# Performance work log

Hardware: AMD Instinct MI355X
Metric: run time of the kernel (lower is better)

The kernel has to match this reference:

```python
import jax, jax.numpy as jnp
import numpy as np

EPS = 1e-7  # SimplifiedLayerNorm eps


def setup_inputs() -> dict:
    key = jax.random.key(0)
    k1, k2 = jax.random.split(key)
    x = jax.random.normal(k1, (8, 2048, 64), dtype=jnp.float32)   # [B, T, d]
    W = jax.random.normal(k2, (2048, 8), dtype=jnp.float32)       # [T, H] per-distance, per-head Toeplitz weights
    return {"x": x, "W": W}


def _l2norm(v):
    return v / (jnp.linalg.norm(v, axis=-1, keepdims=True) + EPS)


def reference(x, W):
    B, T, d = x.shape
    H = W.shape[1]
    # pad one zero token: [B, T+1, d]
    xp = jnp.concatenate([x, jnp.zeros((B, 1, d), x.dtype)], axis=1)
    idx = jnp.arange(T + 1)
    dist = idx[:, None] - idx[None, :]                 # [T+1, T+1], row - col
    # Toeplitz logits: W[dist, h] for 0 <= dist < T; the single dist==T entry
    # (bottom-left corner) is left at its initial 0.0; dist < 0 is causally masked.
    Wd = W[jnp.clip(dist, 0, T - 1)]                   # [T+1, T+1, H]
    dist3 = dist[..., None]
    logits = jnp.where(dist3 < 0, -jnp.inf,
                       jnp.where(dist3 >= T, jnp.zeros((), x.dtype), Wd))
    probs = jax.nn.softmax(logits, axis=1)             # softmax over columns (dim=-1 of W_h)
    v = jnp.einsum('tsh,bsd->hbtd', probs, xp)         # [H, B, T+1, d]
    v = _l2norm(v)
    V = jnp.concatenate([v, xp[None]], axis=0)         # [H+1, B, T+1, d]
    V = _l2norm(V)
    return V
```

## Files before the change

### kernel.cpp

```cpp
#include <hip/hip_runtime.h>

#define EPS 1e-7f
#define T_DIM 2048
#define TP1   2049
#define H_DIM 8
#define B_DIM 8
#define SP    2080
#define NFRAG 134
#define FB_OFF 32
#define RSTRIDE 66

typedef short v8s __attribute__((ext_vector_type(8)));
typedef float v4f __attribute__((ext_vector_type(4)));

static __device__ __forceinline__ unsigned short f2bf(float f) {
  union { float f; unsigned u; } v; v.f = f;
  unsigned r = v.u + 0x7fffu + ((v.u >> 16) & 1u);
  return (unsigned short)(r >> 16);
}

#define J1_BLOCKS 268
#define J2_BLOCKS 264
#define J3_BLOCKS 4098

__global__ __launch_bounds__(256) void prep(const float* __restrict__ x,
                                            const float* __restrict__ W,
                                            unsigned short* __restrict__ fragA,
                                            unsigned short* __restrict__ xT,
                                            float* __restrict__ out) {
  __shared__ float tile[64][65];
  int bid = blockIdx.x;
  if (bid < J1_BLOCKS) {
    int tid = bid * 256 + threadIdx.x;
    int blk = tid >> 6, lane = tid & 63;
    int h = blk / NFRAG, fb = blk - h * NFRAG;
    int b0 = fb * 16 - FB_OFF;
    int lm = lane & 15, quad = lane >> 4;
    v8s frag;
    #pragma unroll
    for (int j = 0; j < 8; ++j) {
      int d = b0 + lm - 8 * quad - j;
      float v = 0.0f;
      if (d >= 0 && d < T_DIM) v = __expf(W[d * H_DIM + h]);
      else if (d == T_DIM) v = 1.0f;
      frag[j] = (short)f2bf(v);
    }
    *(v8s*)(fragA + (size_t)tid * 8) = frag;
    return;
  }
  bid -= J1_BLOCKS;
  if (bid < J2_BLOCKS) {
    int b = bid / 33, st = bid % 33;
    int tid = threadIdx.x;
    if (st == 32) {
      #pragma unroll
      for (int i = 0; i < 8; ++i) {
        int idx = tid * 8 + i;
        int dd = idx >> 5, sl = idx & 31;
        xT[((size_t)b * 64 + dd) * SP + T_DIM + sl] = 0;
      }
      return;
    }
    int s0 = st * 64;
    int c = tid & 63, r4 = tid >> 6;
    #pragma unroll
    for (int i = 0; i < 16; ++i) {
      int sl = r4 * 16 + i;
      tile[sl][c] = x[((size_t)b * T_DIM + (s0 + sl)) * 64 + c];
    }
    __syncthreads();
    #pragma unroll
    for (int i = 0; i < 16; ++i) {
      int dd = r4 * 16 + i;
      xT[((size_t)b * 64 + dd) * SP + s0 + c] = f2bf(tile[c][dd]);
    }
    return;
  }
  bid -= J2_BLOCKS;
  {
    int row = bid * 4 + (threadIdx.x >> 6);
    if (row >= B_DIM * TP1) return;
    int b = row / TP1, t = row - b * TP1;
    int dd = threadIdx.x & 63;
    float v = (t < T_DIM) ? x[((size_t)b * T_DIM + t) * 64 + dd] : 0.0f;
    float ss = v * v;
    ss += __shfl_xor(ss, 1);  ss += __shfl_xor(ss, 2);
    ss += __shfl_xor(ss, 4);  ss += __shfl_xor(ss, 8);
    ss += __shfl_xor(ss, 16); ss += __shfl_xor(ss, 32);
    float inv = 1.0f / (sqrtf(ss) + EPS);
    out[(((size_t)(H_DIM * B_DIM + b) * TP1 + t) << 6) + dd] = v * inv;
  }
}

__global__ __launch_bounds__(256) void toeplitz_mm(const unsigned short* __restrict__ fragA,
                                                   const unsigned short* __restrict__ xT,
                                                   float* __restrict__ out) {
  __shared__ float bufA[64 * RSTRIDE];
  __shared__ float bufB[64 * RSTRIDE];

  const int lane = threadIdx.x & 63;
  const int w    = threadIdx.x >> 6;
  const int lm   = lane & 15;
  const int quad = lane >> 4;

  const int bi  = blockIdx.x;
  const int tt  = 32 - (bi >> 6);
  const int rem = bi & 63;
  const int h = rem >> 3, b = rem & 7;
  const int t0 = tt * 64;

  const unsigned short* fA = fragA + ((size_t)h * NFRAG * 64 + lane) * 8;
  const unsigned short* xb = xT + ((size_t)b * 64 + lm) * SP + 8 * quad;

  const int s_end = min(t0 + 32, T_DIM);

  v4f acc[4][4] = {};

  v8s a0[4], a1[4], b0[4], b1[4];

#define LOAD_A(dst, s0v) do {                                        \
    const v8s* _p = (const v8s*)(fA + (size_t)(((t0 - (s0v) + FB_OFF) >> 4)) * 512); \
    dst[0] = _p[0]; dst[1] = _p[64]; dst[2] = _p[128]; dst[3] = _p[192]; } while (0)
#define LOAD_B(dst, s0v) do {                                        \
    const unsigned short* _p = xb + (s0v);                           \
    dst[0] = *(const v8s*)(_p);                                      \
    dst[1] = *(const v8s*)(_p + 16 * SP);                            \
    dst[2] = *(const v8s*)(_p + 32 * SP);                            \
    dst[3] = *(const v8s*)(_p + 48 * SP); } while (0)
#define DO_MFMA(fa, fb) do {                                         \
    _Pragma("unroll")                                                \
    for (int mt = 0; mt < 4; ++mt)                                   \
      _Pragma("unroll")                                              \
      for (int nt = 0; nt < 4; ++nt)                                 \
        acc[mt][nt] = __builtin_amdgcn_mfma_f32_16x16x32_bf16(fa[mt], fb[nt], acc[mt][nt], 0, 0, 0); } while (0)

  int s0 = 32 * w;
  if (s0 <= s_end) {
    LOAD_A(a0, s0); LOAD_B(b0, s0);
    for (;;) {
      bool more = (s0 + 128 <= s_end);
      if (more) { LOAD_A(a1, s0 + 128); LOAD_B(b1, s0 + 128); }
      DO_MFMA(a0, b0);
      if (!more) break;
      s0 += 128;
      bool more2 = (s0 + 128 <= s_end);
      if (more2) { LOAD_A(a0, s0 + 128); LOAD_B(b0, s0 + 128); }
      DO_MFMA(a1, b1);
      if (!more2) break;
      s0 += 128;
    }
  }

#define ST_ACC(buf) do {                                             \
    _Pragma("unroll")                                                \
    for (int mt = 0; mt < 4; ++mt)                                   \
      _Pragma("unroll")                                              \
      for (int r = 0; r < 4; ++r) {                                  \
        int row = 16 * mt + 4 * quad + r;                            \
        _Pragma("unroll")                                            \
        for (int nt = 0; nt < 4; ++nt)                               \
          buf[row * RSTRIDE + 16 * nt + lm] = acc[mt][nt][r]; } } while (0)
#define ADD_ACC(buf) do {                                            \
    _Pragma("unroll")                                                \
    for (int mt = 0; mt < 4; ++mt)                                   \
      _Pragma("unroll")                                              \
      for (int r = 0; r < 4; ++r) {                                  \
        int row = 16 * mt + 4 * quad + r;                            \
        _Pragma("unroll")                                            \
        for (int nt = 0; nt < 4; ++nt)                               \
          acc[mt][nt][r] += buf[row * RSTRIDE + 16 * nt + lm]; } } while (0)

  if (w == 1) ST_ACC(bufA);
  if (w == 3) ST_ACC(bufB);
  __syncthreads();
  if (w == 0) ADD_ACC(bufA);
  if (w == 2) ADD_ACC(bufB);
  __syncthreads();
  if (w == 2) ST_ACC(bufA);
  __syncthreads();
  if (w != 0) return;
  ADD_ACC(bufA);

  #pragma unroll
  for (int mt = 0; mt < 4; ++mt) {
    #pragma unroll
    for (int r = 0; r < 4; ++r) {
      float ss = 0.0f;
      #pragma unroll
      for (int nt = 0; nt < 4; ++nt) { float a = acc[mt][nt][r]; ss += a * a; }
      ss += __shfl_xor(ss, 1);
      ss += __shfl_xor(ss, 2);
      ss += __shfl_xor(ss, 4);
      ss += __shfl_xor(ss, 8);
      int t = t0 + 16 * mt + 4 * quad + r;
      if (t <= T_DIM) {
        float n1 = sqrtf(ss);
        float u  = n1 / (n1 + EPS);
        float inv = 1.0f / ((n1 + EPS) * (u + EPS));
        float* op = out + (((size_t)(h * B_DIM + b) * TP1 + t) << 6) + lm;
        #pragma unroll
        for (int nt = 0; nt < 4; ++nt) op[16 * nt] = acc[mt][nt][r] * inv;
      }
    }
  }
}

extern "C" void kernel_launch(void* const* d_in, const int* in_sizes, int n_in,
                              void* d_out, int out_size, void* d_ws, size_t ws_size,
                              hipStream_t stream) {
  const float* x = (const float*)d_in[0];
  const float* W = (const float*)d_in[1];
  float* out = (float*)d_out;

  unsigned short* xT    = (unsigned short*)d_ws;
  unsigned short* fragA = (unsigned short*)((char*)d_ws + 2131968);

  hipLaunchKernelGGL(prep, dim3(J1_BLOCKS + J2_BLOCKS + J3_BLOCKS), dim3(256), 0, stream,
                     x, W, fragA, xT, out);
  hipLaunchKernelGGL(toeplitz_mm, dim3(64 * 33), dim3(256), 0, stream, fragA, xT, out);
}
```

Baseline: 119.0 us.

## Split Toeplitz GEMM blocks into 2 row tiles x 2 K-splits with nontemporal stores

Each block now covers 128 output rows. Two waves each own a 64-row tile, and two waves split the K range for each tile, replacing the 4-way K-split and its three-step LDS reduction with a single exchange. The grid halves and the h/b mapping is reordered so that neighbouring blocks share the same x slice. The fragment table grows to cover the larger distance range, and output stores become nontemporal. Each wave now walks a longer K loop, so latency hiding and load balance change.

After: 115.1 us. 3.3% less time.

```diff
diff --git a/kernel.cpp b/kernel.cpp
--- a/kernel.cpp
+++ b/kernel.cpp
@@ -6,7 +6,7 @@
 #define H_DIM 8
 #define B_DIM 8
 #define SP    2080
-#define NFRAG 134
+#define NFRAG 138
 #define FB_OFF 32
 #define RSTRIDE 66
 
@@ -19,7 +19,7 @@
   return (unsigned short)(r >> 16);
 }
 
-#define J1_BLOCKS 268
+#define J1_BLOCKS 276
 #define J2_BLOCKS 264
 #define J3_BLOCKS 4098
 
@@ -88,38 +88,41 @@
     ss += __shfl_xor(ss, 4);  ss += __shfl_xor(ss, 8);
     ss += __shfl_xor(ss, 16); ss += __shfl_xor(ss, 32);
     float inv = 1.0f / (sqrtf(ss) + EPS);
-    out[(((size_t)(H_DIM * B_DIM + b) * TP1 + t) << 6) + dd] = v * inv;
+    __builtin_nontemporal_store(v * inv,
+        &out[(((size_t)(H_DIM * B_DIM + b) * TP1 + t) << 6) + dd]);
   }
 }
 
 __global__ __launch_bounds__(256) void toeplitz_mm(const unsigned short* __restrict__ fragA,
                                                    const unsigned short* __restrict__ xT,
                                                    float* __restrict__ out) {
-  __shared__ float bufA[64 * RSTRIDE];
-  __shared__ float bufB[64 * RSTRIDE];
+  __shared__ float red[2][64 * RSTRIDE];
 
   const int lane = threadIdx.x & 63;
   const int w    = threadIdx.x >> 6;
+  const int wm   = w & 1;
+  const int wk   = w >> 1;
   const int lm   = lane & 15;
   const int quad = lane >> 4;
 
   const int bi  = blockIdx.x;
-  const int tt  = 32 - (bi >> 6);
+  const int tb  = 16 - (bi >> 6);
   const int rem = bi & 63;
-  const int h = rem >> 3, b = rem & 7;
-  const int t0 = tt * 64;
+  const int h = rem & 7, b = (rem >> 3) & 7;
+  const int t0 = tb * 128;
+  const int tw = t0 + 64 * wm;
 
   const unsigned short* fA = fragA + ((size_t)h * NFRAG * 64 + lane) * 8;
   const unsigned short* xb = xT + ((size_t)b * 64 + lm) * SP + 8 * quad;
 
-  const int s_end = min(t0 + 32, T_DIM);
+  const int sw_end = min(tw + 32, T_DIM);
 
   v4f acc[4][4] = {};
 
   v8s a0[4], a1[4], b0[4], b1[4];
 
 #define LOAD_A(dst, s0v) do {                                        \
-    const v8s* _p = (const v8s*)(fA + (size_t)(((t0 - (s0v) + FB_OFF) >> 4)) * 512); \
+    const v8s* _p = (const v8s*)(fA + (size_t)((tw - (s0v) + FB_OFF) >> 4) * 512); \
     dst[0] = _p[0]; dst[1] = _p[64]; dst[2] = _p[128]; dst[3] = _p[192]; } while (0)
 #define LOAD_B(dst, s0v) do {                                        \
     const unsigned short* _p = xb + (s0v);                           \
@@ -134,52 +137,47 @@
       for (int nt = 0; nt < 4; ++nt)                                 \
         acc[mt][nt] = __builtin_amdgcn_mfma_f32_16x16x32_bf16(fa[mt], fb[nt], acc[mt][nt], 0, 0, 0); } while (0)
 
-  int s0 = 32 * w;
-  if (s0 <= s_end) {
-    LOAD_A(a0, s0); LOAD_B(b0, s0);
-    for (;;) {
-      bool more = (s0 + 128 <= s_end);
-      if (more) { LOAD_A(a1, s0 + 128); LOAD_B(b1, s0 + 128); }
-      DO_MFMA(a0, b0);
-      if (!more) break;
-      s0 += 128;
-      bool more2 = (s0 + 128 <= s_end);
-      if (more2) { LOAD_A(a0, s0 + 128); LOAD_B(b0, s0 + 128); }
-      DO_MFMA(a1, b1);
-      if (!more2) break;
-      s0 += 128;
-    }
-  }
-
-#define ST_ACC(buf) do {                                             \
-    _Pragma("unroll")                                                \
-    for (int mt = 0; mt < 4; ++mt)                                   \
-      _Pragma("unroll")                                              \
-      for (int r = 0; r < 4; ++r) {                                  \
-        int row = 16 * mt + 4 * quad + r;                            \
-        _Pragma("unroll")                                            \
-        for (int nt = 0; nt < 4; ++nt)                               \
-          buf[row * RSTRIDE + 16 * nt + lm] = acc[mt][nt][r]; } } while (0)
-#define ADD_ACC(buf) do {                                            \
-    _Pragma("unroll")                                                \
-    for (int mt = 0; mt < 4; ++mt)                                   \
-      _Pragma("unroll")                                              \
-      for (int r = 0; r < 4; ++r) {                                  \
-        int row = 16 * mt + 4 * quad + r;                            \
-        _Pragma("unroll")                                            \
-        for (int nt = 0; nt < 4; ++nt)                               \
-          acc[mt][nt][r] += buf[row * RSTRIDE + 16 * nt + lm]; } } while (0)
-
-  if (w == 1) ST_ACC(bufA);
-  if (w == 3) ST_ACC(bufB);
+  int s0 = 32 * wk;
+  LOAD_A(a0, s0); LOAD_B(b0, s0);
+  for (;;) {
+    bool more = (s0 + 64 <= sw_end);
+    if (more) { LOAD_A(a1, s0 + 64); LOAD_B(b1, s0 + 64); }
+    DO_MFMA(a0, b0);
+    if (!more) break;
+    s0 += 64;
+    bool more2 = (s0 + 64 <= sw_end);
+    if (more2) { LOAD_A(a0, s0 + 64); LOAD_B(b0, s0 + 64); }
+    DO_MFMA(a1, b1);
+    if (!more2) break;
+    s0 += 64;
+  }
+
+  if (wk == 1) {
+    float* buf = red[wm];
+    #pragma unroll
+    for (int mt = 0; mt < 4; ++mt)
+      #pragma unroll
+      for (int r = 0; r < 4; ++r) {
+        int row = 16 * mt + 4 * quad + r;
+        #pragma unroll
+        for (int nt = 0; nt < 4; ++nt)
+          buf[row * RSTRIDE + 16 * nt + lm] = acc[mt][nt][r];
+      }
+  }
   __syncthreads();
-  if (w == 0) ADD_ACC(bufA);
-  if (w == 2) ADD_ACC(bufB);
-  __syncthreads();
-  if (w == 2) ST_ACC(bufA);
-  __syncthreads();
-  if (w != 0) return;
-  ADD_ACC(bufA);
+  if (wk != 0) return;
+
+  const float* buf = red[wm];
+  #pragma unroll
+  for (int mt = 0; mt < 4; ++mt) {
+    #pragma unroll
+    for (int r = 0; r < 4; ++r) {
+      int row = 16 * mt + 4 * quad + r;
+      #pragma unroll
+      for (int nt = 0; nt < 4; ++nt)
+        acc[mt][nt][r] += buf[row * RSTRIDE + 16 * nt + lm];
+    }
+  }
 
   #pragma unroll
   for (int mt = 0; mt < 4; ++mt) {
@@ -192,14 +190,15 @@
       ss += __shfl_xor(ss, 2);
       ss += __shfl_xor(ss, 4);
       ss += __shfl_xor(ss, 8);
-      int t = t0 + 16 * mt + 4 * quad + r;
+      int t = tw + 16 * mt + 4 * quad + r;
       if (t <= T_DIM) {
         float n1 = sqrtf(ss);
         float u  = n1 / (n1 + EPS);
         float inv = 1.0f / ((n1 + EPS) * (u + EPS));
         float* op = out + (((size_t)(h * B_DIM + b) * TP1 + t) << 6) + lm;
         #pragma unroll
-        for (int nt = 0; nt < 4; ++nt) op[16 * nt] = acc[mt][nt][r] * inv;
+        for (int nt = 0; nt < 4; ++nt)
+          __builtin_nontemporal_store(acc[mt][nt][r] * inv, op + 16 * nt);
       }
     }
   }
@@ -217,5 +216,5 @@
 
   hipLaunchKernelGGL(prep, dim3(J1_BLOCKS + J2_BLOCKS + J3_BLOCKS), dim3(256), 0, stream,
                      x, W, fragA, xT, out);
-  hipLaunchKernelGGL(toeplitz_mm, dim3(64 * 33), dim3(256), 0, stream, fragA, xT, out);
-}
+  hipLaunchKernelGGL(toeplitz_mm, dim3(64 * 17), dim3(256), 0, stream, fragA, xT, out);
+}
```
